# Optimization experiments

Hardware: AMD Instinct MI355X
Metric: run time of the kernel (lower is better)

The kernel has to match this reference:

```python
import jax, jax.numpy as jnp
import numpy as np


def setup_inputs() -> dict:
    key = jax.random.key(0)
    k1, k2, k3, k4, k5 = jax.random.split(key, 5)
    B, C, D = 16384, 1000, 2048
    x = jax.random.normal(k1, (B, D), dtype=jnp.float32)
    W = jax.random.normal(k2, (C, D), dtype=jnp.float32) * 0.02  # fc weight
    b = jax.random.normal(k3, (C,), dtype=jnp.float32) * 0.01
    selector_weights = jax.random.normal(k4, (5,), dtype=jnp.float32) * 0.01
    selector_thresholds = jax.random.normal(k5, (5,), dtype=jnp.float32) * 0.01
    ensemble_threshold = jnp.zeros((1,), dtype=jnp.float32)
    return {
        "x": x, "W": W, "b": b,
        "selector_weights": selector_weights,
        "selector_thresholds": selector_thresholds,
        "ensemble_threshold": ensemble_threshold,
    }


def _selector_scores(logits, W):
    # top-2 of raw logits (RLConfM): sorted descending -> top_k(2)
    top2, _ = jax.lax.top_k(logits, 2)
    conf_m = top2[:, 0] - top2[:, 1]
    # geometric margin (RLGeoM): logits normalized by row norms of fc weight
    w_norms = jnp.linalg.norm(W, axis=1)                      # [C]
    norm_logits = logits / (w_norms + 1e-8)[None, :]          # [B, C]
    ntop2, _ = jax.lax.top_k(norm_logits, 2)
    geo_m = ntop2[:, 0] - ntop2[:, 1]
    # softmax-based selectors share one softmax pass
    probs = jax.nn.softmax(logits, axis=1)                    # [B, C]
    sr_max = jnp.max(probs, axis=1)
    doctor = 1.0 - 1.0 / jnp.sum(probs * probs, axis=1)
    neg_entropy = jnp.sum(probs * jnp.log(probs + 1e-10), axis=1)  # = -entropy
    # order matches nn.ModuleList: [SRMax, SRDoctor, SREntropy, RLGeoM, RLConfM]
    return jnp.stack([sr_max, doctor, neg_entropy, geo_m, conf_m], axis=1)  # [B, 5]


def reference(x, W, b, selector_weights, selector_thresholds, ensemble_threshold):
    # base model runs under no_grad in the original
    logits = jax.lax.stop_gradient(jnp.dot(x, W.T) + b)       # [B, C]
    scores = _selector_scores(logits, jax.lax.stop_gradient(W))  # [B, 5]
    indicators = jnp.tanh(scores - selector_thresholds[None, :])  # [B, 5]
    ensemble = jnp.sum(selector_weights[None, :] * indicators, axis=1)  # [B]
    selection_score = jnp.tanh(ensemble - ensemble_threshold[0])
    return (logits, selection_score)
```

## Files before the change

### kernel.cpp

```cpp
#include <hip/hip_runtime.h>
#include <stdint.h>

#define B_ROWS 16384
#define C_COLS 1000
#define D_DIM  2048

typedef __bf16 bf16x8 __attribute__((ext_vector_type(8)));
typedef float  f32x4  __attribute__((ext_vector_type(4)));
typedef unsigned short u16;

__device__ __forceinline__ u16 f2bf(float f) {
  union { float f; uint32_t u; } v; v.f = f;
  return (u16)((v.u + 0x7FFFu + ((v.u >> 16) & 1u)) >> 16);
}

__global__ __launch_bounds__(256)
void prep(const float* __restrict__ W, const float* __restrict__ x,
          u16* __restrict__ Wb, u16* __restrict__ xb, float* __restrict__ norms) {
  const int r = blockIdx.x;
  const int t = threadIdx.x;
  const bool isW = (r < C_COLS);
  const float* src = isW ? (W + (size_t)r * D_DIM)
                         : (x + (size_t)(r - C_COLS) * D_DIM);
  u16* dst = isW ? (Wb + (size_t)r * D_DIM)
                 : (xb + (size_t)(r - C_COLS) * D_DIM);
  const int c = t * 8;
  float4 v0 = *reinterpret_cast<const float4*>(src + c);
  float4 v1 = *reinterpret_cast<const float4*>(src + c + 4);
  uint32_t p0 = (uint32_t)f2bf(v0.x) | ((uint32_t)f2bf(v0.y) << 16);
  uint32_t p1 = (uint32_t)f2bf(v0.z) | ((uint32_t)f2bf(v0.w) << 16);
  uint32_t p2 = (uint32_t)f2bf(v1.x) | ((uint32_t)f2bf(v1.y) << 16);
  uint32_t p3 = (uint32_t)f2bf(v1.z) | ((uint32_t)f2bf(v1.w) << 16);
  const int row_id = isW ? r : (r - C_COLS);
  const int m2 = (row_id & 7) << 3;
  uint4 val; val.x = p0; val.y = p1; val.z = p2; val.w = p3;
  *reinterpret_cast<uint4*>(dst + (c ^ m2)) = val;
  if (isW) {
    float ss = v0.x*v0.x + v0.y*v0.y + v0.z*v0.z + v0.w*v0.w
             + v1.x*v1.x + v1.y*v1.y + v1.z*v1.z + v1.w*v1.w;
    #pragma unroll
    for (int m = 32; m; m >>= 1) ss += __shfl_xor(ss, m);
    __shared__ float wss[4];
    if ((t & 63) == 0) wss[t >> 6] = ss;
    __syncthreads();
    if (t == 0) norms[r] = sqrtf(wss[0] + wss[1] + wss[2] + wss[3]);
  }
}

#define ABASE(B,H) (((B)*2+(H))*8192)
#define BBASE(B,H) (32768 + ((B)*2+(H))*8192)

#define STAGE_A(BUF,H,OFF) { _Pragma("unroll") for (int j_=0;j_<2;++j_){ \
    u16* d_ = lds + ABASE(BUF,H) + (j_*64 + w*8)*64; \
    __builtin_amdgcn_global_load_lds( \
      (const __attribute__((address_space(1))) void*)(sa[H][j_] + (OFF)), \
      (__attribute__((address_space(3))) void*)d_, 16, 0, 0); } }

#define STAGE_B(BUF,H,OFF) { _Pragma("unroll") for (int j_=0;j_<2;++j_){ \
    u16* d_ = lds + BBASE(BUF,H) + (j_*64 + w*8)*64; \
    __builtin_amdgcn_global_load_lds( \
      (const __attribute__((address_space(1))) void*)(sb[H][j_] + (OFF)), \
      (__attribute__((address_space(3))) void*)d_, 16, 0, 0); } }

#define READ_A_KS(BUF,MH,KS) { _Pragma("unroll") for (int fr_=0;fr_<4;++fr_) \
    Acur[KS][fr_] = *reinterpret_cast<const bf16x8*>( \
        pA[KS] + ((BUF)*2+(MH))*16384 + fr_*2048); }

#define READ_B_KS(BUF,NH,DST,KS) { _Pragma("unroll") for (int fc_=0;fc_<2;++fc_) \
    DST[KS][fc_] = *reinterpret_cast<const bf16x8*>( \
        pB[KS] + ((BUF)*2+(NH))*16384 + fc_*2048); }

#define MMAK(MH,NH,BSRC,KS) { \
  _Pragma("unroll") for (int fr_=0;fr_<4;++fr_) \
    _Pragma("unroll") for (int fc_=0;fc_<2;++fc_) \
      acc[MH][fr_][NH][fc_] = __builtin_amdgcn_mfma_f32_16x16x32_bf16( \
          Acur[KS][fr_], BSRC[KS][fc_], acc[MH][fr_][NH][fc_], 0, 0, 0); }

#define BAR   __builtin_amdgcn_s_barrier()
#define LG0   asm volatile("s_waitcnt lgkmcnt(0)" ::: "memory")
#define LGK0  asm volatile("s_waitcnt lgkmcnt(0)" ::: "memory")
#define LGK4  asm volatile("s_waitcnt lgkmcnt(4)" ::: "memory")
#define LGK8  asm volatile("s_waitcnt lgkmcnt(8)" ::: "memory")
#define SCHB  __builtin_amdgcn_sched_barrier(0)
#define VM4   asm volatile("s_waitcnt vmcnt(4)" ::: "memory")
#define VM0   asm volatile("s_waitcnt vmcnt(0)" ::: "memory")
#define SETP1 __builtin_amdgcn_s_setprio(1)
#define SETP0 __builtin_amdgcn_s_setprio(0)

#define SMERGE(m_,s_,q_,u_,om_,os_,oq_,ou_) { \
    float M_ = fmaxf(m_, om_); \
    float a_ = __expf(m_ - M_), b_ = __expf(om_ - M_); \
    float ns_ = a_*s_ + b_*os_; \
    float nq_ = a_*a_*q_ + b_*b_*oq_; \
    float nu_ = a_*(u_ + (m_-M_)*s_) + b_*(ou_ + (om_-M_)*os_); \
    m_ = M_; s_ = ns_; q_ = nq_; u_ = nu_; }

#define T2MERGE(t1_,t2_,o1_,o2_) { \
    if (o1_ > t1_) { t2_ = fmaxf(t1_, o2_); t1_ = o1_; } else t2_ = fmaxf(t2_, o1_); }

template<int FUSE>
__global__ __launch_bounds__(512, 2)
void gemm8(const u16* __restrict__ xb, const u16* __restrict__ Wb,
           const float* __restrict__ bias, float* __restrict__ out,
           const float* __restrict__ norms, float* __restrict__ partials) {
  __shared__ u16 lds[65536];

  const int bid = blockIdx.x;
  const int swz = (bid & 7) * 32 + (bid >> 3);
  const int tm = swz >> 2, tn = swz & 3;
  const int m0 = tm * 256, n0 = tn * 256;

  const int t = threadIdx.x, w = t >> 6, l = t & 63;
  const int wr = w >> 2, wcn = w & 3;

  f32x4 acc[2][4][2][2];
  #pragma unroll
  for (int a = 0; a < 2; ++a)
    #pragma unroll
    for (int b2 = 0; b2 < 4; ++b2)
      #pragma unroll
      for (int c2 = 0; c2 < 2; ++c2)
        #pragma unroll
        for (int d2 = 0; d2 < 2; ++d2)
          acc[a][b2][c2][d2] = (f32x4){0.f, 0.f, 0.f, 0.f};

  bf16x8 Acur[2][4], B0c[2][2], B1c[2][2];

  const char* ldsc = (const char*)lds;
  const int la  = l & 15;
  const int hi3 = (l >> 4) << 3;
  const int m3  = (l & 7) << 3;
  const char* pA[2];
  const char* pB[2];
  pA[0] = ldsc + wr*8192 + la*128 + (((0  + hi3) ^ m3) << 1);
  pA[1] = ldsc + wr*8192 + la*128 + (((32 + hi3) ^ m3) << 1);
  pB[0] = ldsc + 65536 + (wcn*32 + la)*128 + (((0  + hi3) ^ m3) << 1);
  pB[1] = ldsc + 65536 + (wcn*32 + la)*128 + (((32 + hi3) ^ m3) << 1);

  const char* sa[2][2];
  const char* sb[2][2];
  #pragma unroll
  for (int H = 0; H < 2; ++H)
    #pragma unroll
    for (int j = 0; j < 2; ++j) {
      sa[H][j] = (const char*)xb +
        (((size_t)(m0 + H*128 + j*64 + w*8 + (l>>3))) * D_DIM + (l&7)*8) * 2;
      int gr = n0 + H*128 + j*64 + w*8 + (l>>3);
      if (gr >= C_COLS) gr = C_COLS - 1;
      sb[H][j] = (const char*)Wb + ((size_t)gr * D_DIM + (l&7)*8) * 2;
    }

  STAGE_A(0,0,0); STAGE_B(0,0,0); STAGE_A(0,1,0); STAGE_B(0,1,0);
  STAGE_A(1,0,128); STAGE_B(1,0,128);
  VM4;
  BAR;

  for (int it = 0; it < 15; ++it) {
    READ_A_KS(0,0,0); READ_B_KS(0,0,B0c,0); READ_B_KS(0,1,B1c,0);
    READ_A_KS(0,0,1); READ_B_KS(0,0,B0c,1); READ_B_KS(0,1,B1c,1);
    STAGE_A(1,1,128); STAGE_B(1,1,128);
    BAR; LGK8; SETP1; SCHB;
    MMAK(0,0,B0c,0); MMAK(0,1,B1c,0);
    LGK0; SCHB;
    MMAK(0,0,B0c,1); MMAK(0,1,B1c,1); SETP0;
    BAR;
    READ_A_KS(0,1,0); READ_A_KS(0,1,1);
    STAGE_A(0,0,256); STAGE_B(0,0,256);
    BAR; LGK4; SETP1; SCHB;
    MMAK(1,1,B1c,0); MMAK(1,0,B0c,0);
    LGK0; SCHB;
    MMAK(1,1,B1c,1); MMAK(1,0,B0c,1); SETP0;
    VM4; BAR;
    READ_A_KS(1,0,0); READ_B_KS(1,0,B0c,0); READ_B_KS(1,1,B1c,0);
    READ_A_KS(1,0,1); READ_B_KS(1,0,B0c,1); READ_B_KS(1,1,B1c,1);
    STAGE_A(0,1,256); STAGE_B(0,1,256);
    BAR; LGK8; SETP1; SCHB;
    MMAK(0,0,B0c,0); MMAK(0,1,B1c,0);
    LGK0; SCHB;
    MMAK(0,0,B0c,1); MMAK(0,1,B1c,1); SETP0;
    BAR;
    READ_A_KS(1,1,0); READ_A_KS(1,1,1);
    STAGE_A(1,0,384); STAGE_B(1,0,384);
    BAR; LGK4; SETP1; SCHB;
    MMAK(1,1,B1c,0); MMAK(1,0,B0c,0);
    LGK0; SCHB;
    MMAK(1,1,B1c,1); MMAK(1,0,B0c,1); SETP0;
    VM4; BAR;
    #pragma unroll
    for (int H = 0; H < 2; ++H)
      #pragma unroll
      for (int j = 0; j < 2; ++j) { sa[H][j] += 256; sb[H][j] += 256; }
  }
  READ_A_KS(0,0,0); READ_B_KS(0,0,B0c,0); READ_B_KS(0,1,B1c,0);
  READ_A_KS(0,0,1); READ_B_KS(0,0,B0c,1); READ_B_KS(0,1,B1c,1);
  STAGE_A(1,1,128); STAGE_B(1,1,128);
  BAR; LGK8; SETP1; SCHB;
  MMAK(0,0,B0c,0); MMAK(0,1,B1c,0);
  LGK0; SCHB;
  MMAK(0,0,B0c,1); MMAK(0,1,B1c,1); SETP0;
  BAR;
  READ_A_KS(0,1,0); READ_A_KS(0,1,1);
  BAR; LGK4; SETP1; SCHB;
  MMAK(1,1,B1c,0); MMAK(1,0,B0c,0);
  LGK0; SCHB;
  MMAK(1,1,B1c,1); MMAK(1,0,B0c,1); SETP0;
  VM0; BAR;
  READ_A_KS(1,0,0); READ_B_KS(1,0,B0c,0); READ_B_KS(1,1,B1c,0);
  READ_A_KS(1,0,1); READ_B_KS(1,0,B0c,1); READ_B_KS(1,1,B1c,1);
  BAR; LGK8; SETP1; SCHB;
  MMAK(0,0,B0c,0); MMAK(0,1,B1c,0);
  LGK0; SCHB;
  MMAK(0,0,B0c,1); MMAK(0,1,B1c,1); SETP0;
  BAR;
  READ_A_KS(1,1,0); READ_A_KS(1,1,1);
  BAR; LGK4; SETP1; SCHB;
  MMAK(1,1,B1c,0); MMAK(1,0,B0c,0);
  LGK0; SCHB;
  MMAK(1,1,B1c,1); MMAK(1,0,B0c,1); SETP0;

  float bv[2][2]; bool okc[2][2];
  #pragma unroll
  for (int nh = 0; nh < 2; ++nh)
    #pragma unroll
    for (int fc = 0; fc < 2; ++fc) {
      int col = n0 + nh*128 + wcn*32 + fc*16 + (l & 15);
      okc[nh][fc] = (col < C_COLS);
      bv[nh][fc]  = okc[nh][fc] ? bias[col] : 0.f;
    }

  if constexpr (!FUSE) {
    #pragma unroll
    for (int mh = 0; mh < 2; ++mh)
      #pragma unroll
      for (int nh = 0; nh < 2; ++nh)
        #pragma unroll
        for (int fc = 0; fc < 2; ++fc)
          if (okc[nh][fc]) {
            int col = n0 + nh*128 + wcn*32 + fc*16 + (l & 15);
            #pragma unroll
            for (int fr = 0; fr < 4; ++fr) {
              int row0 = m0 + mh*128 + wr*64 + fr*16 + ((l >> 4) << 2);
              #pragma unroll
              for (int j = 0; j < 4; ++j)
                out[(size_t)(row0 + j) * C_COLS + col] = acc[mh][fr][nh][fc][j] + bv[nh][fc];
            }
          }
  }

  if constexpr (FUSE) {
    float* sf = (float*)lds;
    const int rrow = t >> 2;
    const int q    = t & 3;
    BAR;
    #pragma unroll
    for (int mh = 0; mh < 2; ++mh) {
      #pragma unroll
      for (int fr = 0; fr < 4; ++fr)
        #pragma unroll
        for (int j = 0; j < 4; ++j) {
          int rl = wr*64 + fr*16 + ((l >> 4) << 2) + j;
          int sw = (rl & 7) << 2;
          #pragma unroll
          for (int nh = 0; nh < 2; ++nh)
            #pragma unroll
            for (int fc = 0; fc < 2; ++fc) {
              int c = nh*128 + wcn*32 + fc*16 + (l & 15);
              sf[rl*256 + (c ^ sw)] = acc[mh][fr][nh][fc][j] + bv[nh][fc];
            }
        }
      LG0; BAR;
      float m=-3.4e38f, t1=-3.4e38f, t2=-3.4e38f, n1=-3.4e38f, n2=-3.4e38f;
      #pragma unroll
      for (int i = 0; i < 16; ++i) {
        int U = i*4 + q;
        f32x4 v4 = *reinterpret_cast<const f32x4*>(
            &sf[rrow*256 + 4*(U ^ (rrow & 7))]);
        f32x4 w4 = *reinterpret_cast<const f32x4*>(&norms[n0 + 4*U]);
        if (n0 + 4*U + 3 < C_COLS)
          *reinterpret_cast<f32x4*>(
              &out[(size_t)(m0 + mh*128 + rrow) * C_COLS + n0 + 4*U]) = v4;
        #pragma unroll
        for (int e = 0; e < 4; ++e) {
          int col = n0 + 4*U + e;
          if (col < C_COLS) {
            float v = v4[e];
            m = fmaxf(m, v);
            if (v > t1) { t2 = t1; t1 = v; } else if (v > t2) t2 = v;
            float nv = v / (w4[e] + 1e-8f);
            if (nv > n1) { n2 = n1; n1 = nv; } else if (nv > n2) n2 = nv;
          }
        }
      }
      float s = 0.f, qq = 0.f, u = 0.f;
      #pragma unroll
      for (int i = 0; i < 16; ++i) {
        int U = i*4 + q;
        f32x4 v4 = *reinterpret_cast<const f32x4*>(
            &sf[rrow*256 + 4*(U ^ (rrow & 7))]);
        #pragma unroll
        for (int e = 0; e < 4; ++e) {
          int col = n0 + 4*U + e;
          if (col < C_COLS) {
            float d = v4[e] - m;
            float ee = __expf(d);
            s += ee; qq += ee*ee; u += d*ee;
          }
        }
      }
      LG0;
      #pragma unroll
      for (int msk = 1; msk < 4; msk <<= 1) {
        float o1 = __shfl_xor(t1, msk), o2 = __shfl_xor(t2, msk);
        T2MERGE(t1, t2, o1, o2);
        float p1 = __shfl_xor(n1, msk), p2 = __shfl_xor(n2, msk);
        T2MERGE(n1, n2, p1, p2);
        float om = __shfl_xor(m, msk), os = __shfl_xor(s, msk);
        float oq = __shfl_xor(qq, msk), ou = __shfl_xor(u, msk);
        SMERGE(m, s, qq, u, om, os, oq, ou);
      }
      if (q == 0) {
        float* pp = partials + ((size_t)(m0 + mh*128 + rrow) * 4 + tn) * 8;
        float4 lo; lo.x=t1; lo.y=t2; lo.z=n1; lo.w=n2;
        float4 hi; hi.x=m;  hi.y=s;  hi.z=qq; hi.w=u;
        *reinterpret_cast<float4*>(pp)     = lo;
        *reinterpret_cast<float4*>(pp + 4) = hi;
      }
      if (mh == 0) { BAR; }
    }
  }
}

__global__ __launch_bounds__(256)
void selector2(const float* __restrict__ partials,
               const float* __restrict__ selw, const float* __restrict__ selt,
               const float* __restrict__ ethr, float* __restrict__ out2) {
  const int row = blockIdx.x * 256 + threadIdx.x;
  const float* pp = partials + (size_t)row * 32;
  float P[4][8];
  #pragma unroll
  for (int wv = 0; wv < 4; ++wv) {
    float4 lo = *reinterpret_cast<const float4*>(pp + wv*8);
    float4 hi = *reinterpret_cast<const float4*>(pp + wv*8 + 4);
    P[wv][0]=lo.x; P[wv][1]=lo.y; P[wv][2]=lo.z; P[wv][3]=lo.w;
    P[wv][4]=hi.x; P[wv][5]=hi.y; P[wv][6]=hi.z; P[wv][7]=hi.w;
  }
  float t1=P[0][0], t2=P[0][1], n1=P[0][2], n2=P[0][3];
  float m=P[0][4], s=P[0][5], q=P[0][6], u=P[0][7];
  #pragma unroll
  for (int wv = 1; wv < 4; ++wv) {
    T2MERGE(t1, t2, P[wv][0], P[wv][1]);
    T2MERGE(n1, n2, P[wv][2], P[wv][3]);
    SMERGE(m, s, q, u, P[wv][4], P[wv][5], P[wv][6], P[wv][7]);
  }
  float sc0 = 1.f / s;
  float sc1 = 1.f - (s * s) / q;
  float sc2 = u / s - __logf(s);
  float sc3 = n1 - n2;
  float sc4 = t1 - t2;
  float ens = selw[0] * tanhf(sc0 - selt[0])
            + selw[1] * tanhf(sc1 - selt[1])
            + selw[2] * tanhf(sc2 - selt[2])
            + selw[3] * tanhf(sc3 - selt[3])
            + selw[4] * tanhf(sc4 - selt[4]);
  out2[row] = tanhf(ens - ethr[0]);
}

__global__ __launch_bounds__(256)
void selector(const float* __restrict__ logits, const float* __restrict__ norms,
              const float* __restrict__ selw, const float* __restrict__ selt,
              const float* __restrict__ ethr, float* __restrict__ out) {
  __shared__ float nrm[1024];
  const int t = threadIdx.x;
  #pragma unroll
  for (int i = 0; i < 4; ++i) {
    int idx = t + i * 256;
    nrm[idx] = (idx < C_COLS) ? norms[idx] : 1.0f;
  }
  __syncthreads();
  const int w = t >> 6, l = t & 63;
  const int row = blockIdx.x * 4 + w;
  const float* lp = logits + (size_t)row * C_COLS;
  float lg[16];
  float t1 = -3.4e38f, t2 = -3.4e38f, n1 = -3.4e38f, n2 = -3.4e38f;
  #pragma unroll
  for (int i = 0; i < 4; ++i) {
    float4 v4 = *reinterpret_cast<const float4*>(lp + l * 4 + i * 256);
    #pragma unroll
    for (int j = 0; j < 4; ++j) {
      int idx = l * 4 + i * 256 + j;
      float raw = (j == 0) ? v4.x : (j == 1) ? v4.y : (j == 2) ? v4.z : v4.w;
      bool ok = (idx < C_COLS);
      float v = ok ? raw : -3.4e38f;
      lg[i * 4 + j] = v;
      if (v > t1) { t2 = t1; t1 = v; } else if (v > t2) t2 = v;
      float nv = ok ? raw / (nrm[idx] + 1e-8f) : -3.4e38f;
      if (nv > n1) { n2 = n1; n1 = nv; } else if (nv > n2) n2 = nv;
    }
  }
  #pragma unroll
  for (int m = 1; m < 64; m <<= 1) {
    float o1 = __shfl_xor(t1, m), o2 = __shfl_xor(t2, m);
    T2MERGE(t1, t2, o1, o2);
    float p1 = __shfl_xor(n1, m), p2 = __shfl_xor(n2, m);
    T2MERGE(n1, n2, p1, p2);
  }
  const float mx = t1;
  float S = 0.f, sq = 0.f;
  float ex[16];
  #pragma unroll
  for (int i = 0; i < 16; ++i) {
    float e = (lg[i] > -1e38f) ? __expf(lg[i] - mx) : 0.f;
    ex[i] = e; S += e; sq += e * e;
  }
  #pragma unroll
  for (int m = 1; m < 64; m <<= 1) { S += __shfl_xor(S, m); sq += __shfl_xor(sq, m); }
  float ent = 0.f;
  #pragma unroll
  for (int i = 0; i < 16; ++i)
    if (lg[i] > -1e38f) { float p = ex[i] / S; ent += p * __logf(p + 1e-10f); }
  #pragma unroll
  for (int m = 1; m < 64; m <<= 1) ent += __shfl_xor(ent, m);
  if (l == 0) {
    float ens = selw[0] * tanhf(1.f / S - selt[0])
              + selw[1] * tanhf(1.f - (S * S) / sq - selt[1])
              + selw[2] * tanhf(ent - selt[2])
              + selw[3] * tanhf(n1 - n2 - selt[3])
              + selw[4] * tanhf(t1 - t2 - selt[4]);
    out[row] = tanhf(ens - ethr[0]);
  }
}

extern "C" void kernel_launch(void* const* d_in, const int* in_sizes, int n_in,
                              void* d_out, int out_size, void* d_ws, size_t ws_size,
                              hipStream_t stream) {
  const float* x    = (const float*)d_in[0];
  const float* W    = (const float*)d_in[1];
  const float* b    = (const float*)d_in[2];
  const float* selw = (const float*)d_in[3];
  const float* selt = (const float*)d_in[4];
  const float* ethr = (const float*)d_in[5];
  float* out = (float*)d_out;
  float* out2 = out + (size_t)B_ROWS * C_COLS;

  u16*   Wb    = (u16*)d_ws;
  float* norms = (float*)((char*)d_ws + 4096000);
  u16*   xb    = (u16*)((char*)d_ws + 4100096);
  float* parts = (float*)((char*)d_ws + 4100096 + 67108864);

  const size_t need_fuse = 4100096 + 67108864 + 2097152;
  const size_t need_r4   = 4100096 + 67108864;

  if (ws_size >= need_fuse) {
    prep<<<C_COLS + B_ROWS, 256, 0, stream>>>(W, x, Wb, xb, norms);
    gemm8<1><<<256, 512, 0, stream>>>(xb, Wb, b, out, norms, parts);
    selector2<<<B_ROWS / 256, 256, 0, stream>>>(parts, selw, selt, ethr, out2);
  } else if (ws_size >= need_r4) {
    prep<<<C_COLS + B_ROWS, 256, 0, stream>>>(W, x, Wb, xb, norms);
    gemm8<0><<<256, 512, 0, stream>>>(xb, Wb, b, out, norms, nullptr);
    selector<<<B_ROWS / 4, 256, 0, stream>>>(out, norms, selw, selt, ethr, out2);
  }
}
```

Measured before the change: 117.3 us.

## Fuse fp32-to-bf16 conversion of x into GEMM A-tile staging

The separate prep pass that converted all of x to bf16 in workspace is removed. The GEMM now loads fp32 x directly into registers, converts to bf16 and writes swizzled tiles to LDS, with a deeper register prefetch pipeline (two float4 sets, vmcnt adjusted). This removes a full read/write of the 128MB-scale x conversion and its workspace, at the cost of more registers, VGPR-mediated LDS writes instead of direct global-to-LDS loads, and twice the global bytes per A tile inside the GEMM (each x tile is re-read by the 4 column tiles).

```diff
diff --git a/kernel.cpp b/kernel.cpp
--- a/kernel.cpp
+++ b/kernel.cpp
@@ -15,46 +15,46 @@
 }
 
 __global__ __launch_bounds__(256)
-void prep(const float* __restrict__ W, const float* __restrict__ x,
-          u16* __restrict__ Wb, u16* __restrict__ xb, float* __restrict__ norms) {
+void prep_w(const float* __restrict__ W, u16* __restrict__ Wb,
+            float* __restrict__ norms) {
   const int r = blockIdx.x;
   const int t = threadIdx.x;
-  const bool isW = (r < C_COLS);
-  const float* src = isW ? (W + (size_t)r * D_DIM)
-                         : (x + (size_t)(r - C_COLS) * D_DIM);
-  u16* dst = isW ? (Wb + (size_t)r * D_DIM)
-                 : (xb + (size_t)(r - C_COLS) * D_DIM);
+  const float* row = W + (size_t)r * D_DIM;
   const int c = t * 8;
-  float4 v0 = *reinterpret_cast<const float4*>(src + c);
-  float4 v1 = *reinterpret_cast<const float4*>(src + c + 4);
+  float4 v0 = *reinterpret_cast<const float4*>(row + c);
+  float4 v1 = *reinterpret_cast<const float4*>(row + c + 4);
+  float ss = v0.x*v0.x + v0.y*v0.y + v0.z*v0.z + v0.w*v0.w
+           + v1.x*v1.x + v1.y*v1.y + v1.z*v1.z + v1.w*v1.w;
   uint32_t p0 = (uint32_t)f2bf(v0.x) | ((uint32_t)f2bf(v0.y) << 16);
   uint32_t p1 = (uint32_t)f2bf(v0.z) | ((uint32_t)f2bf(v0.w) << 16);
   uint32_t p2 = (uint32_t)f2bf(v1.x) | ((uint32_t)f2bf(v1.y) << 16);
   uint32_t p3 = (uint32_t)f2bf(v1.z) | ((uint32_t)f2bf(v1.w) << 16);
-  const int row_id = isW ? r : (r - C_COLS);
-  const int m2 = (row_id & 7) << 3;
+  const int mask = (r & 7) << 3;
   uint4 val; val.x = p0; val.y = p1; val.z = p2; val.w = p3;
-  *reinterpret_cast<uint4*>(dst + (c ^ m2)) = val;
-  if (isW) {
-    float ss = v0.x*v0.x + v0.y*v0.y + v0.z*v0.z + v0.w*v0.w
-             + v1.x*v1.x + v1.y*v1.y + v1.z*v1.z + v1.w*v1.w;
-    #pragma unroll
-    for (int m = 32; m; m >>= 1) ss += __shfl_xor(ss, m);
-    __shared__ float wss[4];
-    if ((t & 63) == 0) wss[t >> 6] = ss;
-    __syncthreads();
-    if (t == 0) norms[r] = sqrtf(wss[0] + wss[1] + wss[2] + wss[3]);
-  }
+  *reinterpret_cast<uint4*>(Wb + (size_t)r * D_DIM + (c ^ mask)) = val;
+  #pragma unroll
+  for (int m = 32; m; m >>= 1) ss += __shfl_xor(ss, m);
+  __shared__ float wss[4];
+  if ((t & 63) == 0) wss[t >> 6] = ss;
+  __syncthreads();
+  if (t == 0) norms[r] = sqrtf(wss[0] + wss[1] + wss[2] + wss[3]);
 }
 
 #define ABASE(B,H) (((B)*2+(H))*8192)
 #define BBASE(B,H) (32768 + ((B)*2+(H))*8192)
 
-#define STAGE_A(BUF,H,OFF) { _Pragma("unroll") for (int j_=0;j_<2;++j_){ \
-    u16* d_ = lds + ABASE(BUF,H) + (j_*64 + w*8)*64; \
-    __builtin_amdgcn_global_load_lds( \
-      (const __attribute__((address_space(1))) void*)(sa[H][j_] + (OFF)), \
-      (__attribute__((address_space(3))) void*)d_, 16, 0, 0); } }
+#define ISSUE_A(SET,H,OFF) { _Pragma("unroll") for (int j_=0;j_<2;++j_){ \
+    const float* s_ = (const float*)(xa[H][j_] + (OFF)); \
+    SET[2*j_]   = *reinterpret_cast<const float4*>(s_); \
+    SET[2*j_+1] = *reinterpret_cast<const float4*>(s_ + 4); } }
+
+#define WRITE_A(SET,BUF,H) { _Pragma("unroll") for (int j_=0;j_<2;++j_){ \
+    bf16x8 h_; \
+    h_[0]=(__bf16)SET[2*j_].x;   h_[1]=(__bf16)SET[2*j_].y; \
+    h_[2]=(__bf16)SET[2*j_].z;   h_[3]=(__bf16)SET[2*j_].w; \
+    h_[4]=(__bf16)SET[2*j_+1].x; h_[5]=(__bf16)SET[2*j_+1].y; \
+    h_[6]=(__bf16)SET[2*j_+1].z; h_[7]=(__bf16)SET[2*j_+1].w; \
+    *reinterpret_cast<bf16x8*>(wA + ((BUF)*2+(H))*16384 + j_*8192) = h_; } }
 
 #define STAGE_B(BUF,H,OFF) { _Pragma("unroll") for (int j_=0;j_<2;++j_){ \
     u16* d_ = lds + BBASE(BUF,H) + (j_*64 + w*8)*64; \
@@ -82,7 +82,7 @@
 #define LGK4  asm volatile("s_waitcnt lgkmcnt(4)" ::: "memory")
 #define LGK8  asm volatile("s_waitcnt lgkmcnt(8)" ::: "memory")
 #define SCHB  __builtin_amdgcn_sched_barrier(0)
-#define VM4   asm volatile("s_waitcnt vmcnt(4)" ::: "memory")
+#define VM6   asm volatile("s_waitcnt vmcnt(6)" ::: "memory")
 #define VM0   asm volatile("s_waitcnt vmcnt(0)" ::: "memory")
 #define SETP1 __builtin_amdgcn_s_setprio(1)
 #define SETP0 __builtin_amdgcn_s_setprio(0)
@@ -100,7 +100,7 @@
 
 template<int FUSE>
 __global__ __launch_bounds__(512, 2)
-void gemm8(const u16* __restrict__ xb, const u16* __restrict__ Wb,
+void gemm8(const float* __restrict__ x, const u16* __restrict__ Wb,
            const float* __restrict__ bias, float* __restrict__ out,
            const float* __restrict__ norms, float* __restrict__ partials) {
   __shared__ u16 lds[65536];
@@ -125,6 +125,7 @@
           acc[a][b2][c2][d2] = (f32x4){0.f, 0.f, 0.f, 0.f};
 
   bf16x8 Acur[2][4], B0c[2][2], B1c[2][2];
+  float4 set0[4], set1[4];
 
   const char* ldsc = (const char*)lds;
   const int la  = l & 15;
@@ -137,63 +138,75 @@
   pB[0] = ldsc + 65536 + (wcn*32 + la)*128 + (((0  + hi3) ^ m3) << 1);
   pB[1] = ldsc + 65536 + (wcn*32 + la)*128 + (((32 + hi3) ^ m3) << 1);
 
-  const char* sa[2][2];
+  char* wA = (char*)lds + (w*8 + (l>>3))*128
+           + ((((l&7)*8) ^ (((l>>3)&7)<<3)) << 1);
+
+  const char* xa[2][2];
   const char* sb[2][2];
   #pragma unroll
   for (int H = 0; H < 2; ++H)
     #pragma unroll
     for (int j = 0; j < 2; ++j) {
-      sa[H][j] = (const char*)xb +
-        (((size_t)(m0 + H*128 + j*64 + w*8 + (l>>3))) * D_DIM + (l&7)*8) * 2;
+      xa[H][j] = (const char*)x +
+        (((size_t)(m0 + H*128 + j*64 + w*8 + (l>>3))) * D_DIM + (l&7)*8) * 4;
       int gr = n0 + H*128 + j*64 + w*8 + (l>>3);
       if (gr >= C_COLS) gr = C_COLS - 1;
       sb[H][j] = (const char*)Wb + ((size_t)gr * D_DIM + (l&7)*8) * 2;
     }
 
-  STAGE_A(0,0,0); STAGE_B(0,0,0); STAGE_A(0,1,0); STAGE_B(0,1,0);
-  STAGE_A(1,0,128); STAGE_B(1,0,128);
-  VM4;
+  ISSUE_A(set0, 0, 0);   WRITE_A(set0, 0, 0);
+  ISSUE_A(set0, 1, 0);   WRITE_A(set0, 0, 1);
+  ISSUE_A(set0, 0, 256); WRITE_A(set0, 1, 0);
+  STAGE_B(0,0,0); STAGE_B(0,1,0); STAGE_B(1,0,128);
+  ISSUE_A(set0, 1, 256);
+  ISSUE_A(set1, 0, 512);
+  VM0; LG0;
   BAR;
 
   for (int it = 0; it < 15; ++it) {
+    WRITE_A(set0, 1, 1);
     READ_A_KS(0,0,0); READ_B_KS(0,0,B0c,0); READ_B_KS(0,1,B1c,0);
     READ_A_KS(0,0,1); READ_B_KS(0,0,B0c,1); READ_B_KS(0,1,B1c,1);
-    STAGE_A(1,1,128); STAGE_B(1,1,128);
+    ISSUE_A(set0, 1, 512); STAGE_B(1,1,128);
     BAR; LGK8; SETP1; SCHB;
     MMAK(0,0,B0c,0); MMAK(0,1,B1c,0);
     LGK0; SCHB;
     MMAK(0,0,B0c,1); MMAK(0,1,B1c,1); SETP0;
     BAR;
+    WRITE_A(set1, 0, 0);
     READ_A_KS(0,1,0); READ_A_KS(0,1,1);
-    STAGE_A(0,0,256); STAGE_B(0,0,256);
+    ISSUE_A(set1, 0, 768); STAGE_B(0,0,256);
     BAR; LGK4; SETP1; SCHB;
     MMAK(1,1,B1c,0); MMAK(1,0,B0c,0);
     LGK0; SCHB;
     MMAK(1,1,B1c,1); MMAK(1,0,B0c,1); SETP0;
-    VM4; BAR;
+    VM6; BAR;
+    WRITE_A(set0, 0, 1);
     READ_A_KS(1,0,0); READ_B_KS(1,0,B0c,0); READ_B_KS(1,1,B1c,0);
     READ_A_KS(1,0,1); READ_B_KS(1,0,B0c,1); READ_B_KS(1,1,B1c,1);
-    STAGE_A(0,1,256); STAGE_B(0,1,256);
+    ISSUE_A(set0, 1, 768); STAGE_B(0,1,256);
     BAR; LGK8; SETP1; SCHB;
     MMAK(0,0,B0c,0); MMAK(0,1,B1c,0);
     LGK0; SCHB;
     MMAK(0,0,B0c,1); MMAK(0,1,B1c,1); SETP0;
     BAR;
+    WRITE_A(set1, 1, 0);
     READ_A_KS(1,1,0); READ_A_KS(1,1,1);
-    STAGE_A(1,0,384); STAGE_B(1,0,384);
+    ISSUE_A(set1, 0, (it < 14) ? 1024 : 512); STAGE_B(1,0,384);
     BAR; LGK4; SETP1; SCHB;
     MMAK(1,1,B1c,0); MMAK(1,0,B0c,0);
     LGK0; SCHB;
     MMAK(1,1,B1c,1); MMAK(1,0,B0c,1); SETP0;
-    VM4; BAR;
+    VM6; BAR;
     #pragma unroll
     for (int H = 0; H < 2; ++H)
       #pragma unroll
-      for (int j = 0; j < 2; ++j) { sa[H][j] += 256; sb[H][j] += 256; }
-  }
+      for (int j = 0; j < 2; ++j) { xa[H][j] += 512; sb[H][j] += 256; }
+  }
+  WRITE_A(set0, 1, 1);
   READ_A_KS(0,0,0); READ_B_KS(0,0,B0c,0); READ_B_KS(0,1,B1c,0);
   READ_A_KS(0,0,1); READ_B_KS(0,0,B0c,1); READ_B_KS(0,1,B1c,1);
-  STAGE_A(1,1,128); STAGE_B(1,1,128);
+  STAGE_B(1,1,128);
   BAR; LGK8; SETP1; SCHB;
   MMAK(0,0,B0c,0); MMAK(0,1,B1c,0);
   LGK0; SCHB;
@@ -444,19 +457,16 @@
 
   u16*   Wb    = (u16*)d_ws;
   float* norms = (float*)((char*)d_ws + 4096000);
-  u16*   xb    = (u16*)((char*)d_ws + 4100096);
-  float* parts = (float*)((char*)d_ws + 4100096 + 67108864);
-
-  const size_t need_fuse = 4100096 + 67108864 + 2097152;
-  const size_t need_r4   = 4100096 + 67108864;
-
+  float* parts = (float*)((char*)d_ws + 4100096);
+
+  const size_t need_fuse = 4100096 + 2097152;
+
+  prep_w<<<C_COLS, 256, 0, stream>>>(W, Wb, norms);
   if (ws_size >= need_fuse) {
-    prep<<<C_COLS + B_ROWS, 256, 0, stream>>>(W, x, Wb, xb, norms);
-    gemm8<1><<<256, 512, 0, stream>>>(xb, Wb, b, out, norms, parts);
+    gemm8<1><<<256, 512, 0, stream>>>(x, Wb, b, out, norms, parts);
     selector2<<<B_ROWS / 256, 256, 0, stream>>>(parts, selw, selt, ethr, out2);
-  } else if (ws_size >= need_r4) {
-    prep<<<C_COLS + B_ROWS, 256, 0, stream>>>(W, x, Wb, xb, norms);
-    gemm8<0><<<256, 512, 0, stream>>>(xb, Wb, b, out, norms, nullptr);
+  } else {
+    gemm8<0><<<256, 512, 0, stream>>>(x, Wb, b, out, norms, nullptr);
     selector<<<B_ROWS / 4, 256, 0, stream>>>(out, norms, selw, selt, ethr, out2);
   }
 }
```

After: 163.0 us. 1.39x slower.
